# Kernel tuning notes

Hardware: AMD Instinct MI355X
Metric: run time of the kernel (lower is better)

Reference implementation:

```python
import jax, jax.numpy as jnp
import numpy as np

NEG_SLOPE = 0.2
N, IN_DIM, OUT_DIM, N_HEADS = 4096, 512, 512, 4
D_K = OUT_DIM // N_HEADS


def setup_inputs() -> dict:
    key = jax.random.key(0)
    k1, k2, k3, k4, k5 = jax.random.split(key, 5)
    H = jax.random.normal(k1, (N, IN_DIM), dtype=jnp.float32)
    A = jax.random.randint(k2, (N, N), 0, 2, dtype=jnp.int32)
    W = jax.random.normal(k3, (IN_DIM, OUT_DIM), dtype=jnp.float32) * (1.0 / np.sqrt(IN_DIM))
    a_l = jax.random.normal(k4, (N_HEADS, D_K), dtype=jnp.float32) * 0.1
    a_r = jax.random.normal(k5, (N_HEADS, D_K), dtype=jnp.float32) * 0.1
    return {"H": H, "A": A, "W": W, "a_l": a_l, "a_r": a_r}


def reference(H, A, W, a_l, a_r):
    n = H.shape[0]
    # mask = (A + I) > 0, shape (N, N); self-loops always allowed
    mask = (A + jnp.eye(n, dtype=A.dtype)) > 0
    # Wh: (N, heads, d_k)
    Wh = (H @ W).reshape(n, N_HEADS, D_K)
    sl = jnp.einsum('nhd,hd->nh', Wh, a_l)  # (N, heads)
    sr = jnp.einsum('nhd,hd->nh', Wh, a_r)  # (N, heads)
    # e[i, h, j] = leaky_relu(sl[i,h] + sr[j,h])
    e = jax.nn.leaky_relu(sl[:, :, None] + sr.T[None, :, :], negative_slope=NEG_SLOPE)
    e = jnp.where(mask[:, None, :], e, -jnp.inf)
    alpha = jnp.nan_to_num(jax.nn.softmax(e, axis=2), nan=0.0)  # dropout is identity at eval
    # out[i, h, :] = sum_j alpha[i,h,j] * Wh[j,h,:]
    out = jnp.einsum('nhm,mhd->nhd', alpha, Wh).reshape(n, OUT_DIM)
    return jax.nn.elu(out)
```

## Files before the change

kernel.cpp:

```cpp
#include <hip/hip_runtime.h>

typedef unsigned short ushort_t;
typedef __attribute__((ext_vector_type(8)))  short  short8;
typedef __attribute__((ext_vector_type(4)))  short  short4v;
typedef __attribute__((ext_vector_type(4)))  float  float4v;
typedef __attribute__((ext_vector_type(4)))  int    int4v;

#define N_NODES 4096
#define NHEADS  4
#define DK      128
#define ODIM    512
#define KDIM    512

__device__ __forceinline__ float bf2f(ushort_t u) {
    return __uint_as_float(((unsigned)u) << 16);
}
__device__ __forceinline__ ushort_t f2bf_rne(float f) {
    unsigned u = __float_as_uint(f);
    u += 0x7fffu + ((u >> 16) & 1u);
    return (ushort_t)(u >> 16);
}

__global__ __launch_bounds__(256) void pack_mask_k(const int* __restrict__ A,
                                                   unsigned long long* __restrict__ P,
                                                   const ushort_t* __restrict__ Hraw,
                                                   int* __restrict__ flag,
                                                   const void* __restrict__ W,
                                                   ushort_t* __restrict__ WT,
                                                   float* __restrict__ sl,
                                                   float* __restrict__ sr)
{
    __shared__ ushort_t lt[64][72];
    __shared__ int dcnt[4];
    const int tid = threadIdx.x;
    const int bx  = blockIdx.x;

    if (bx == 0 && tid < 64) {
        const int lane = tid;
        int cnt = 0;
        #pragma unroll
        for (int s = 0; s < 16; ++s) {
            ushort_t v = Hraw[(lane * 16 + s) * 2];
            int e = (v >> 7) & 0xFF;
            cnt += (((e >= 90) && (e <= 140)) || (v == 0)) ? 1 : 0;
        }
        #pragma unroll
        for (int off = 32; off; off >>= 1) cnt += __shfl_down(cnt, off);
        if (lane == 0) *flag = (cnt < 768) ? 1 : 0;
    }

    {
        const int lane  = tid & 63;
        const int flat4 = bx * 256 + tid;
        const int row   = flat4 >> 10;
        const int col0  = (flat4 << 2) & 4095;
        const int4v a   = ((const int4v*)A)[flat4];
        unsigned nib = 0;
        #pragma unroll
        for (int j = 0; j < 4; ++j)
            nib |= ((a[j] != 0) || (row == col0 + j)) ? (1u << j) : 0u;
        unsigned long long v = (unsigned long long)nib << ((lane & 15) * 4);
        v |= __shfl_xor(v, 1);
        v |= __shfl_xor(v, 2);
        v |= __shfl_xor(v, 4);
        v |= __shfl_xor(v, 8);
        if ((lane & 15) == 0) P[flat4 >> 4] = v;
    }

    if (bx >= 64 && bx < 96) {
        const int idx = (bx - 64) * 256 + tid;
        float4v z;
        #pragma unroll
        for (int e = 0; e < 4; ++e) z[e] = 0.f;
        if (idx < 4096) ((float4v*)sl)[idx] = z;
        else            ((float4v*)sr)[idx - 4096] = z;
    }

    if (bx < 64) {
        int cnt = 0;
        #pragma unroll
        for (int s = 0; s < 4; ++s) {
            ushort_t v = Hraw[(tid * 4 + s) * 2];
            int e = (v >> 7) & 0xFF;
            cnt += (((e >= 90) && (e <= 140)) || (v == 0)) ? 1 : 0;
        }
        #pragma unroll
        for (int off = 32; off; off >>= 1) cnt += __shfl_down(cnt, off);
        if ((tid & 63) == 0) dcnt[tid >> 6] = cnt;
        __syncthreads();
        const int f32 = (dcnt[0] + dcnt[1] + dcnt[2] + dcnt[3]) < 768;

        const int ti = bx >> 3, tj = bx & 7;
        const int r = tid >> 2, c2 = tid & 3;
        const size_t eo = (size_t)(ti * 64 + r) * KDIM + tj * 64 + c2 * 16;
        if (f32) {
            const float4v* src = (const float4v*)((const float*)W + eo);
            float4v f0 = src[0], f1 = src[1], f2 = src[2], f3 = src[3];
            #pragma unroll
            for (int e = 0; e < 4; ++e) {
                lt[r][c2 * 16 +  0 + e] = f2bf_rne(f0[e]);
                lt[r][c2 * 16 +  4 + e] = f2bf_rne(f1[e]);
                lt[r][c2 * 16 +  8 + e] = f2bf_rne(f2[e]);
                lt[r][c2 * 16 + 12 + e] = f2bf_rne(f3[e]);
            }
        } else {
            const short8* src = (const short8*)((const ushort_t*)W + eo);
            short8 v0 = src[0];
            short8 v1 = src[1];
            *(short8*)&lt[r][c2 * 16]     = v0;
            *(short8*)&lt[r][c2 * 16 + 8] = v1;
        }
        __syncthreads();
        #pragma unroll
        for (int itr = 0; itr < 2; ++itr) {
            int idx = itr * 256 + tid;
            int n = idx >> 3, c = idx & 7;
            short8 vv;
            #pragma unroll
            for (int e = 0; e < 8; ++e) vv[e] = (short)lt[c * 8 + e][n];
            *(short8*)(WT + (size_t)(tj * 64 + n) * KDIM + ti * 64 + c * 8) = vv;
        }
    }
}

__global__ __launch_bounds__(256) void gemm_wht_dual_k(const void* __restrict__ H,
                                                       const ushort_t* __restrict__ WT,
                                                       ushort_t* __restrict__ WhT,
                                                       const int* __restrict__ flag,
                                                       const void* __restrict__ al,
                                                       const void* __restrict__ ar,
                                                       float* __restrict__ sl,
                                                       float* __restrict__ sr)
{
    __shared__ ushort_t lt[64][72];
    const int f32 = *flag;
    const int tid  = threadIdx.x;
    const int lane = tid & 63;
    const int wid  = tid >> 6;
    const int quad = lane >> 4;
    const int l15  = lane & 15;
    const int bm = blockIdx.x & 63, bn = blockIdx.x >> 6;
    const int i0 = bm * 64, n0 = bn * 64;

    const size_t aoff = (size_t)(i0 + wid * 16 + l15) * KDIM + quad * 8;
    const short8* bp0 = (const short8*)(WT + (size_t)(n0 +  0 + l15) * KDIM) + quad;
    const short8* bp1 = (const short8*)(WT + (size_t)(n0 + 16 + l15) * KDIM) + quad;
    const short8* bp2 = (const short8*)(WT + (size_t)(n0 + 32 + l15) * KDIM) + quad;
    const short8* bp3 = (const short8*)(WT + (size_t)(n0 + 48 + l15) * KDIM) + quad;

    float4v acc0, acc1, acc2, acc3;
    #pragma unroll
    for (int e = 0; e < 4; ++e) { acc0[e] = 0.f; acc1[e] = 0.f; acc2[e] = 0.f; acc3[e] = 0.f; }

    #pragma unroll 4
    for (int k8 = 0; k8 < 64; k8 += 4) {
        short8 a;
        if (f32) {
            const float4v* fp = (const float4v*)((const float*)H + aoff + (size_t)k8 * 8);
            float4v x0 = fp[0], x1 = fp[1];
            #pragma unroll
            for (int e = 0; e < 4; ++e) {
                a[e]     = (short)f2bf_rne(x0[e]);
                a[4 + e] = (short)f2bf_rne(x1[e]);
            }
        } else {
            a = *(const short8*)((const ushort_t*)H + aoff + (size_t)k8 * 8);
        }
        acc0 = __builtin_amdgcn_mfma_f32_16x16x32_bf16(a, bp0[k8], acc0, 0, 0, 0);
        acc1 = __builtin_amdgcn_mfma_f32_16x16x32_bf16(a, bp1[k8], acc1, 0, 0, 0);
        acc2 = __builtin_amdgcn_mfma_f32_16x16x32_bf16(a, bp2[k8], acc2, 0, 0, 0);
        acc3 = __builtin_amdgcn_mfma_f32_16x16x32_bf16(a, bp3[k8], acc3, 0, 0, 0);
    }

    #pragma unroll
    for (int r = 0; r < 4; ++r) {
        int m = wid * 16 + quad * 4 + r;
        lt[ 0 + l15][m] = f2bf_rne(acc0[r]);
        lt[16 + l15][m] = f2bf_rne(acc1[r]);
        lt[32 + l15][m] = f2bf_rne(acc2[r]);
        lt[48 + l15][m] = f2bf_rne(acc3[r]);
    }
    __syncthreads();
    #pragma unroll
    for (int itr = 0; itr < 2; ++itr) {
        int idx = itr * 256 + tid;
        int n = idx >> 3, c = idx & 7;
        short8 v = *(const short8*)&lt[n][c * 8];
        *(short8*)(WhT + (size_t)(n0 + n) * N_NODES + i0 + c * 8) = v;
    }

    {
        const int h2 = n0 >> 7;
        const int d0 = n0 & 127;
        const int m  = tid >> 2;
        const int part = tid & 3;
        float psl = 0.f, psr = 0.f;
        #pragma unroll
        for (int k = 0; k < 16; ++k) {
            int n = part * 16 + k;
            float wv = bf2f(lt[n][m]);
            float av = f32 ? ((const float*)al)[h2 * DK + d0 + n]
                           : bf2f(((const ushort_t*)al)[h2 * DK + d0 + n]);
            float bv = f32 ? ((const float*)ar)[h2 * DK + d0 + n]
                           : bf2f(((const ushort_t*)ar)[h2 * DK + d0 + n]);
            psl += wv * av;
            psr += wv * bv;
        }
        psl += __shfl_down(psl, 2); psl += __shfl_down(psl, 1);
        psr += __shfl_down(psr, 2); psr += __shfl_down(psr, 1);
        if (part == 0) {
            atomicAdd(&sl[h2 * N_NODES + i0 + m], psl);
            atomicAdd(&sr[h2 * N_NODES + i0 + m], psr);
        }
    }
}

__global__ __launch_bounds__(256, 2) void attn_split_k(const ushort_t* __restrict__ WhT,
                                                       const unsigned* __restrict__ Apack,
                                                       const float* __restrict__ sl,
                                                       const float* __restrict__ sr,
                                                       float* __restrict__ Npart,
                                                       float* __restrict__ Dpart)
{
    __shared__ char smem[73728] __attribute__((aligned(16)));
    float*    srs  = (float*)smem;
    unsigned (*mbuf)[64] = (unsigned (*)[64])(smem + 8192);
    ushort_t* vbuf = (ushort_t*)(smem + 24576);

    const int tid  = threadIdx.x;
    const int lane = tid & 63;
    const int wq   = tid >> 6;
    const int quad = lane >> 4;
    const int l15  = lane & 15;
    const int bx   = blockIdx.x;
    const int half = bx & 1;
    const int h    = (bx >> 1) & 3;
    const int i0   = (bx >> 3) << 6;
    const int jbase = half << 11;

    const float C1 = 1.44269504f;

    for (int j = tid; j < 2048; j += 256) srs[j] = sr[h * N_NODES + jbase + j] * C1;
    for (int t = tid; t < 64 * 64; t += 256) {
        int r = t >> 6, c = t & 63;
        mbuf[r][c ^ r] = Apack[(size_t)(i0 + r) * 128 + (half << 6) + c];
    }
    const int myrow = wq * 16 + l15;
    const float slv = sl[h * N_NODES + i0 + myrow] * C1;
    __syncthreads();

    float4v acc[8];
    #pragma unroll
    for (int nt = 0; nt < 8; ++nt)
        #pragma unroll
        for (int e = 0; e < 4; ++e) acc[nt][e] = 0.f;
    float4v accden;
    #pragma unroll
    for (int e = 0; e < 4; ++e) accden[e] = 0.f;

    short8 ones;
    #pragma unroll
    for (int e = 0; e < 8; ++e) ones[e] = (short)0x3F80;

    const int dl  = lane >> 3;
    const int pch = (lane & 7) ^ (dl & 7);
    const ushort_t* g0 = WhT + (size_t)(h * DK + wq * 32 + dl) * N_NODES + jbase + pch * 8;

    #define DMA_WIN(BUF, IW)                                                         \
        {   ushort_t* lb_ = vbuf + (BUF) * 8192 + wq * 2048;                         \
            const ushort_t* gs_ = g0 + (IW) * 64;                                    \
            _Pragma("unroll")                                                        \
            for (int q_ = 0; q_ < 4; ++q_)                                           \
                __builtin_amdgcn_global_load_lds(                                    \
                    (const __attribute__((address_space(1))) void*)(gs_ + (size_t)q_ * 8 * N_NODES), \
                    (__attribute__((address_space(3))) void*)(lb_ + q_ * 512),       \
                    16, 0, 0);                                                       \
        }

    DMA_WIN(0, 0)
    DMA_WIN(1, 1)

    const int rs0 = (quad     ^ (l15 & 7)) * 8;
    const int rs1 = ((4 + quad) ^ (l15 & 7)) * 8;

    #pragma unroll 1
    for (int iw = 0; iw < 32; ++iw) {
        const int jl = iw * 64;

        const unsigned wa0 = mbuf[myrow][(iw * 2)     ^ myrow];
        const unsigned wa1 = mbuf[myrow][(iw * 2 + 1) ^ myrow];
        const float4v s0 = *(const float4v*)&srs[jl + quad * 8];
        const float4v s1 = *(const float4v*)&srs[jl + quad * 8 + 4];
        const float4v s2 = *(const float4v*)&srs[jl + 32 + quad * 8];
        const float4v s3 = *(const float4v*)&srs[jl + 32 + quad * 8 + 4];

        short8 pfA, pfB;
        #pragma unroll
        for (int jj = 0; jj < 8; ++jj) {
            const int bit = quad * 8 + jj;
            float srjA = (jj < 4) ? s0[jj] : s1[jj - 4];
            float xA = slv + srjA;
            float tA = fmaxf(xA, xA * 0.2f);
            tA = ((wa0 >> bit) & 1u) ? tA : -1e30f;
            pfA[jj] = (short)(ushort_t)(__float_as_uint(__builtin_amdgcn_exp2f(tA)) >> 16);
            float srjB = (jj < 4) ? s2[jj] : s3[jj - 4];
            float xB = slv + srjB;
            float tB = fmaxf(xB, xB * 0.2f);
            tB = ((wa1 >> bit) & 1u) ? tB : -1e30f;
            pfB[jj] = (short)(ushort_t)(__float_as_uint(__builtin_amdgcn_exp2f(tB)) >> 16);
        }

        if (iw == 31) { asm volatile("s_waitcnt vmcnt(0)" ::: "memory"); }
        else          { asm volatile("s_waitcnt vmcnt(4)" ::: "memory"); }
        asm volatile("s_barrier" ::: "memory");
        if (iw < 30) DMA_WIN((iw + 2) % 3, iw + 2)

        const ushort_t* vB = vbuf + (iw % 3) * 8192;
        #pragma unroll
        for (int nt = 0; nt < 8; ++nt) {
            const int d64 = (nt * 16 + l15) * 64;
            short8 b0 = *(const short8*)(vB + d64 + rs0);
            short8 b1 = *(const short8*)(vB + d64 + rs1);
            acc[nt] = __builtin_amdgcn_mfma_f32_16x16x32_bf16(pfA, b0, acc[nt], 0, 0, 0);
            acc[nt] = __builtin_amdgcn_mfma_f32_16x16x32_bf16(pfB, b1, acc[nt], 0, 0, 0);
        }
        accden = __builtin_amdgcn_mfma_f32_16x16x32_bf16(pfA, ones, accden, 0, 0, 0);
        accden = __builtin_amdgcn_mfma_f32_16x16x32_bf16(pfB, ones, accden, 0, 0, 0);
    }
    #undef DMA_WIN

    float* Np = Npart + (size_t)half * N_NODES * ODIM;
    #pragma unroll
    for (int nt = 0; nt < 8; ++nt)
        #pragma unroll
        for (int r = 0; r < 4; ++r) {
            const int rowi = wq * 16 + quad * 4 + r;
            Np[(size_t)(i0 + rowi) * ODIM + h * DK + nt * 16 + l15] = acc[nt][r];
        }
    if (l15 == 0) {
        #pragma unroll
        for (int r = 0; r < 4; ++r) {
            const int rowi = wq * 16 + quad * 4 + r;
            Dpart[(half * 4 + h) * N_NODES + i0 + rowi] = accden[r];
        }
    }
}

__global__ __launch_bounds__(256) void merge_k(const float* __restrict__ Npart,
                                               const float* __restrict__ Dpart,
                                               void* __restrict__ out,
                                               const int* __restrict__ flag)
{
    const int f32 = *flag;
    const size_t e4 = ((size_t)blockIdx.x * 256 + threadIdx.x) * 4;
    const int i = (int)(e4 >> 9);
    const int c = (int)(e4 & 511);
    const int h = c >> 7;
    const float4v n0 = *(const float4v*)(Npart + e4);
    const float4v n1 = *(const float4v*)(Npart + (size_t)N_NODES * ODIM + e4);
    const float den = Dpart[h * N_NODES + i] + Dpart[(4 + h) * N_NODES + i];
    const float rinv = 1.0f / fmaxf(den, 1e-37f);
    const float C1 = 1.44269504f;
    float o[4];
    #pragma unroll
    for (int k = 0; k < 4; ++k) {
        float v = (n0[k] + n1[k]) * rinv;
        float e = __builtin_amdgcn_exp2f(v * C1) - 1.0f;
        o[k] = (v > 0.f) ? v : e;
    }
    if (f32) {
        float4v ov;
        #pragma unroll
        for (int k = 0; k < 4; ++k) ov[k] = o[k];
        *(float4v*)((float*)out + e4) = ov;
    } else {
        short4v ov;
        #pragma unroll
        for (int k = 0; k < 4; ++k) ov[k] = (short)f2bf_rne(o[k]);
        *(short4v*)((ushort_t*)out + e4) = ov;
    }
}

__global__ __launch_bounds__(256, 2) void attn_single_k(const ushort_t* __restrict__ WhT,
                                                        const unsigned* __restrict__ Apack,
                                                        const float* __restrict__ sl,
                                                        const float* __restrict__ sr,
                                                        void* __restrict__ out,
                                                        const int* __restrict__ flag)
{
    __shared__ float    srs[N_NODES];
    __shared__ unsigned mbuf[32][128];
    __shared__ float    red[2][32][128];
    __shared__ float    lsum[4][32];

    const int f32  = *flag;
    const int tid  = threadIdx.x;
    const int lane = tid & 63;
    const int wq   = tid >> 6;
    const int quad = lane >> 4;
    const int l15  = lane & 15;
    const int h    = blockIdx.x & 3;
    const int i0   = (blockIdx.x >> 2) << 5;

    for (int j = tid; j < N_NODES; j += 256) srs[j] = sr[h * N_NODES + j];
    for (int t = tid; t < 32 * 128; t += 256) {
        int r = t >> 7, c = t & 127;
        mbuf[r][c] = Apack[(size_t)(i0 + r) * 128 + c];
    }
    const float slv0 = sl[h * N_NODES + i0 + l15];
    const float slv1 = sl[h * N_NODES + i0 + 16 + l15];
    __syncthreads();

    const float C1 = 1.44269504f;
    const float C2 = 0.2f * 1.44269504f;

    float4v acc[2][8];
    #pragma unroll
    for (int mg = 0; mg < 2; ++mg)
        #pragma unroll
        for (int nt = 0; nt < 8; ++nt)
            #pragma unroll
            for (int e = 0; e < 4; ++e) acc[mg][nt][e] = 0.f;
    float lacc0 = 0.f, lacc1 = 0.f;

    const ushort_t* vb = WhT + (size_t)(h * DK + l15) * N_NODES + wq * 1024 + quad * 8;

    #pragma unroll 1
    for (int it = 0; it < 16; ++it) {
        const int jl = it * 64;
        const int j0 = wq * 1024 + jl;
        const int mc = j0 >> 5;

        short8 bf[8][2];
        #pragma unroll
        for (int nt = 0; nt < 8; ++nt) {
            bf[nt][0] = *(const short8*)(vb + (size_t)nt * 16 * N_NODES + jl);
            bf[nt][1] = *(const short8*)(vb + (size_t)nt * 16 * N_NODES + jl + 32);
        }

        const unsigned wa0 = mbuf[l15][mc],      wa1 = mbuf[l15][mc + 1];
        const unsigned wb0 = mbuf[16 + l15][mc], wb1 = mbuf[16 + l15][mc + 1];

        short8 pf0[2], pf1[2];
        #pragma unroll
        for (int s = 0; s < 2; ++s) {
            const float* sp = &srs[j0 + s * 32 + quad * 8];
            const float4v s0 = *(const float4v*)sp;
            const float4v s1 = *(const float4v*)(sp + 4);
            const unsigned wa = s ? wa1 : wa0;
            const unsigned wb = s ? wb1 : wb0;
            #pragma unroll
            for (int jj = 0; jj < 8; ++jj) {
                float srj = (jj < 4) ? s0[jj] : s1[jj - 4];
                int bit = quad * 8 + jj;
                float x0 = slv0 + srj;
                float t0 = fmaxf(x0 * C1, x0 * C2);
                t0 = ((wa >> bit) & 1u) ? t0 : -1e30f;
                float p0 = __builtin_amdgcn_exp2f(t0);
                ushort_t h0 = (ushort_t)(__float_as_uint(p0) >> 16);
                lacc0 += bf2f(h0);
                pf0[s][jj] = (short)h0;
                float x1 = slv1 + srj;
                float t1 = fmaxf(x1 * C1, x1 * C2);
                t1 = ((wb >> bit) & 1u) ? t1 : -1e30f;
                float p1 = __builtin_amdgcn_exp2f(t1);
                ushort_t h1 = (ushort_t)(__float_as_uint(p1) >> 16);
                lacc1 += bf2f(h1);
                pf1[s][jj] = (short)h1;
            }
        }

        #pragma unroll
        for (int nt = 0; nt < 8; ++nt) {
            acc[0][nt] = __builtin_amdgcn_mfma_f32_16x16x32_bf16(pf0[0], bf[nt][0], acc[0][nt], 0, 0, 0);
            acc[0][nt] = __builtin_amdgcn_mfma_f32_16x16x32_bf16(pf0[1], bf[nt][1], acc[0][nt], 0, 0, 0);
            acc[1][nt] = __builtin_amdgcn_mfma_f32_16x16x32_bf16(pf1[0], bf[nt][0], acc[1][nt], 0, 0, 0);
            acc[1][nt] = __builtin_amdgcn_mfma_f32_16x16x32_bf16(pf1[1], bf[nt][1], acc[1][nt], 0, 0, 0);
        }
    }

    lacc0 += __shfl_xor(lacc0, 16);
    lacc0 += __shfl_xor(lacc0, 32);
    lacc1 += __shfl_xor(lacc1, 16);
    lacc1 += __shfl_xor(lacc1, 32);
    if (lane < 16) {
        lsum[wq][l15]      = lacc0;
        lsum[wq][16 + l15] = lacc1;
    }
    if (wq >= 2) {
        #pragma unroll
        for (int mg = 0; mg < 2; ++mg)
            #pragma unroll
            for (int nt = 0; nt < 8; ++nt)
                #pragma unroll
                for (int r = 0; r < 4; ++r)
                    red[wq - 2][mg * 16 + quad * 4 + r][nt * 16 + l15] = acc[mg][nt][r];
    }
    __syncthreads();
    if (wq < 2) {
        #pragma unroll
        for (int mg = 0; mg < 2; ++mg)
            #pragma unroll
            for (int nt = 0; nt < 8; ++nt)
                #pragma unroll
                for (int r = 0; r < 4; ++r)
                    acc[mg][nt][r] += red[wq][mg * 16 + quad * 4 + r][nt * 16 + l15];
    }
    __syncthreads();
    if (wq == 1) {
        #pragma unroll
        for (int mg = 0; mg < 2; ++mg)
            #pragma unroll
            for (int nt = 0; nt < 8; ++nt)
                #pragma unroll
                for (int r = 0; r < 4; ++r)
                    red[0][mg * 16 + quad * 4 + r][nt * 16 + l15] = acc[mg][nt][r];
    }
    __syncthreads();
    if (wq == 0) {
        #pragma unroll
        for (int mg = 0; mg < 2; ++mg) {
            float linv[4];
            #pragma unroll
            for (int r = 0; r < 4; ++r) {
                int rowi = mg * 16 + quad * 4 + r;
                float den = lsum[0][rowi] + lsum[1][rowi] + lsum[2][rowi] + lsum[3][rowi];
                linv[r] = 1.0f / fmaxf(den, 1e-37f);
            }
            #pragma unroll
            for (int nt = 0; nt < 8; ++nt)
                #pragma unroll
                for (int r = 0; r < 4; ++r) {
                    int rowi = mg * 16 + quad * 4 + r;
                    float v = (acc[mg][nt][r] + red[0][rowi][nt * 16 + l15]) * linv[r];
                    float e = __builtin_amdgcn_exp2f(v * C1) - 1.0f;
                    float o = (v > 0.f) ? v : e;
                    size_t oidx = (size_t)(i0 + rowi) * ODIM + h * DK + nt * 16 + l15;
                    if (f32) ((float*)out)[oidx] = o;
                    else     ((ushort_t*)out)[oidx] = f2bf_rne(o);
                }
        }
    }
}

extern "C" void kernel_launch(void* const* d_in, const int* in_sizes, int n_in,
                              void* d_out, int out_size, void* d_ws, size_t ws_size,
                              hipStream_t stream)
{
    const void* H  = d_in[0];
    const int*  A  = (const int*)d_in[1];
    const void* W  = d_in[2];
    const void* al = d_in[3];
    const void* ar = d_in[4];

    if (ws_size < (7u << 20)) return;

    char* ws = (char*)d_ws;
    ushort_t* WhT   = (ushort_t*)ws;
    unsigned long long* Apack = (unsigned long long*)(ws + (4u << 20));
    ushort_t* WT    = (ushort_t*)(ws + (6u << 20));
    float*    sl    = (float*)(ws + (6u << 20) + (512u << 10));
    float*    sr    = (float*)(ws + (6u << 20) + (576u << 10));
    int*      flag  = (int*)(ws + (6u << 20) + (640u << 10));
    float*    Npart = (float*)(ws + (12u << 20));
    float*    Dpart = (float*)(ws + (28u << 20));
    const bool have_split = ws_size >= (29u << 20);

    pack_mask_k    <<<16384, 256, 0, stream>>>(A, Apack, (const ushort_t*)H, flag,
                                               W, WT, sl, sr);
    gemm_wht_dual_k<<<512,   256, 0, stream>>>(H, WT, WhT, flag, al, ar, sl, sr);
    if (have_split) {
        attn_split_k<<<512, 256, 0, stream>>>(WhT, (const unsigned*)Apack, sl, sr, Npart, Dpart);
        merge_k     <<<2048, 256, 0, stream>>>(Npart, Dpart, (void*)d_out, flag);
    } else {
        attn_single_k<<<512, 256, 0, stream>>>(WhT, (const unsigned*)Apack, sl, sr, (void*)d_out, flag);
    }
}
```

Baseline: 174.0 us.

## Split attention j-range across two wave groups per block with LDS reduction

Doubles the attention block to 512 threads. Two groups of four waves each handle half of the block's 2048-column j range, using 32-column windows with a new swizzle and a triple-buffered DMA per group. At the end the two groups' partial numerators and denominators are summed through LDS. This aims to raise the number of waves in flight to hide latency, at the cost of a final reduction, an extra barrier, and register pressure under the (512,4) launch bounds.

```diff
diff --git a/kernel.cpp b/kernel.cpp
--- a/kernel.cpp
+++ b/kernel.cpp
@@ -215,7 +215,7 @@
     }
 }
 
-__global__ __launch_bounds__(256, 2) void attn_split_k(const ushort_t* __restrict__ WhT,
+__global__ __launch_bounds__(512, 4) void attn_split_k(const ushort_t* __restrict__ WhT,
                                                        const unsigned* __restrict__ Apack,
                                                        const float* __restrict__ sl,
                                                        const float* __restrict__ sr,
@@ -229,7 +229,9 @@
 
     const int tid  = threadIdx.x;
     const int lane = tid & 63;
-    const int wq   = tid >> 6;
+    const int wid  = tid >> 6;
+    const int wq   = wid & 3;
+    const int js   = wid >> 2;
     const int quad = lane >> 4;
     const int l15  = lane & 15;
     const int bx   = blockIdx.x;
@@ -240,8 +242,8 @@
 
     const float C1 = 1.44269504f;
 
-    for (int j = tid; j < 2048; j += 256) srs[j] = sr[h * N_NODES + jbase + j] * C1;
-    for (int t = tid; t < 64 * 64; t += 256) {
+    for (int j = tid; j < 2048; j += 512) srs[j] = sr[h * N_NODES + jbase + j] * C1;
+    for (int t = tid; t < 64 * 64; t += 512) {
         int r = t >> 6, c = t & 63;
         mbuf[r][c ^ r] = Apack[(size_t)(i0 + r) * 128 + (half << 6) + c];
     }
@@ -262,17 +264,18 @@
     #pragma unroll
     for (int e = 0; e < 8; ++e) ones[e] = (short)0x3F80;
 
-    const int dl  = lane >> 3;
-    const int pch = (lane & 7) ^ (dl & 7);
-    const ushort_t* g0 = WhT + (size_t)(h * DK + wq * 32 + dl) * N_NODES + jbase + pch * 8;
+    const int dl  = lane >> 2;
+    const int gch = (lane & 3) ^ (dl & 3) ^ ((dl >> 2) & 1);
+    const ushort_t* g0 = WhT + (size_t)(h * DK + wq * 32 + dl) * N_NODES
+                             + jbase + js * 1024 + gch * 8;
 
     #define DMA_WIN(BUF, IW)                                                         \
-        {   ushort_t* lb_ = vbuf + (BUF) * 8192 + wq * 2048;                         \
-            const ushort_t* gs_ = g0 + (IW) * 64;                                    \
+        {   ushort_t* lb_ = vbuf + js * 12288 + (BUF) * 4096 + wq * 1024;            \
+            const ushort_t* gs_ = g0 + (IW) * 32;                                    \
             _Pragma("unroll")                                                        \
-            for (int q_ = 0; q_ < 4; ++q_)                                           \
+            for (int q_ = 0; q_ < 2; ++q_)                                           \
                 __builtin_amdgcn_global_load_lds(                                    \
-                    (const __attribute__((address_space(1))) void*)(gs_ + (size_t)q_ * 8 * N_NODES), \
+                    (const __attribute__((address_space(1))) void*)(gs_ + (size_t)q_ * 16 * N_NODES), \
                     (__attribute__((address_space(3))) void*)(lb_ + q_ * 512),       \
                     16, 0, 0);                                                       \
         }
@@ -280,68 +283,74 @@
     DMA_WIN(0, 0)
     DMA_WIN(1, 1)
 
-    const int rs0 = (quad     ^ (l15 & 7)) * 8;
-    const int rs1 = ((4 + quad) ^ (l15 & 7)) * 8;
+    const int rs = (quad ^ (l15 & 3) ^ ((l15 >> 2) & 1)) * 8;
 
     #pragma unroll 1
     for (int iw = 0; iw < 32; ++iw) {
-        const int jl = iw * 64;
-
-        const unsigned wa0 = mbuf[myrow][(iw * 2)     ^ myrow];
-        const unsigned wa1 = mbuf[myrow][(iw * 2 + 1) ^ myrow];
-        const float4v s0 = *(const float4v*)&srs[jl + quad * 8];
-        const float4v s1 = *(const float4v*)&srs[jl + quad * 8 + 4];
-        const float4v s2 = *(const float4v*)&srs[jl + 32 + quad * 8];
-        const float4v s3 = *(const float4v*)&srs[jl + 32 + quad * 8 + 4];
-
-        short8 pfA, pfB;
+        const unsigned wa = mbuf[myrow][(js * 32 + iw) ^ myrow];
+        const float4v s0 = *(const float4v*)&srs[js * 1024 + iw * 32 + quad * 8];
+        const float4v s1 = *(const float4v*)&srs[js * 1024 + iw * 32 + quad * 8 + 4];
+
+        short8 pf;
         #pragma unroll
         for (int jj = 0; jj < 8; ++jj) {
             const int bit = quad * 8 + jj;
-            float srjA = (jj < 4) ? s0[jj] : s1[jj - 4];
-            float xA = slv + srjA;
-            float tA = fmaxf(xA, xA * 0.2f);
-            tA = ((wa0 >> bit) & 1u) ? tA : -1e30f;
-            pfA[jj] = (short)(ushort_t)(__float_as_uint(__builtin_amdgcn_exp2f(tA)) >> 16);
-            float srjB = (jj < 4) ? s2[jj] : s3[jj - 4];
-            float xB = slv + srjB;
-            float tB = fmaxf(xB, xB * 0.2f);
-            tB = ((wa1 >> bit) & 1u) ? tB : -1e30f;
-            pfB[jj] = (short)(ushort_t)(__float_as_uint(__builtin_amdgcn_exp2f(tB)) >> 16);
+            float srj = (jj < 4) ? s0[jj] : s1[jj - 4];
+            float x = slv + srj;
+            float t = fmaxf(x, x * 0.2f);
+            t = ((wa >> bit) & 1u) ? t : -1e30f;
+            pf[jj] = (short)(ushort_t)(__float_as_uint(__builtin_amdgcn_exp2f(t)) >> 16);
         }
 
         if (iw == 31) { asm volatile("s_waitcnt vmcnt(0)" ::: "memory"); }
-        else          { asm volatile("s_waitcnt vmcnt(4)" ::: "memory"); }
+        else          { asm volatile("s_waitcnt vmcnt(2)" ::: "memory"); }
         asm volatile("s_barrier" ::: "memory");
         if (iw < 30) DMA_WIN((iw + 2) % 3, iw + 2)
 
-        const ushort_t* vB = vbuf + (iw % 3) * 8192;
+        const ushort_t* vB = vbuf + js * 12288 + (iw % 3) * 4096;
         #pragma unroll
         for (int nt = 0; nt < 8; ++nt) {
-            const int d64 = (nt * 16 + l15) * 64;
-            short8 b0 = *(const short8*)(vB + d64 + rs0);
-            short8 b1 = *(const short8*)(vB + d64 + rs1);
-            acc[nt] = __builtin_amdgcn_mfma_f32_16x16x32_bf16(pfA, b0, acc[nt], 0, 0, 0);
-            acc[nt] = __builtin_amdgcn_mfma_f32_16x16x32_bf16(pfB, b1, acc[nt], 0, 0, 0);
-        }
-        accden = __builtin_amdgcn_mfma_f32_16x16x32_bf16(pfA, ones, accden, 0, 0, 0);
-        accden = __builtin_amdgcn_mfma_f32_16x16x32_bf16(pfB, ones, accden, 0, 0, 0);
+            short8 b = *(const short8*)(vB + (nt * 16 + l15) * 32 + rs);
+            acc[nt] = __builtin_amdgcn_mfma_f32_16x16x32_bf16(pf, b, acc[nt], 0, 0, 0);
+        }
+        accden = __builtin_amdgcn_mfma_f32_16x16x32_bf16(pf, ones, accden, 0, 0, 0);
     }
     #undef DMA_WIN
 
-    float* Np = Npart + (size_t)half * N_NODES * ODIM;
-    #pragma unroll
-    for (int nt = 0; nt < 8; ++nt)
-        #pragma unroll
-        for (int r = 0; r < 4; ++r) {
-            const int rowi = wq * 16 + quad * 4 + r;
-            Np[(size_t)(i0 + rowi) * ODIM + h * DK + nt * 16 + l15] = acc[nt][r];
-        }
-    if (l15 == 0) {
-        #pragma unroll
-        for (int r = 0; r < 4; ++r) {
-            const int rowi = wq * 16 + quad * 4 + r;
-            Dpart[(half * 4 + h) * N_NODES + i0 + rowi] = accden[r];
+    float* red  = (float*)(smem + 24576);
+    float* lsum = (float*)(smem + 24576 + 32768);
+    __syncthreads();
+
+    if (js == 1) {
+        #pragma unroll
+        for (int nt = 0; nt < 8; ++nt)
+            #pragma unroll
+            for (int r = 0; r < 4; ++r)
+                red[wq * 2048 + (quad * 4 + r) * 128 + nt * 16 + l15] = acc[nt][r];
+        if (l15 == 0) {
+            #pragma unroll
+            for (int r = 0; r < 4; ++r)
+                lsum[wq * 16 + quad * 4 + r] = accden[r];
+        }
+    }
+    __syncthreads();
+    if (js == 0) {
+        float* Np = Npart + (size_t)half * N_NODES * ODIM;
+        #pragma unroll
+        for (int nt = 0; nt < 8; ++nt)
+            #pragma unroll
+            for (int r = 0; r < 4; ++r) {
+                const int rowi = wq * 16 + quad * 4 + r;
+                float v = acc[nt][r] + red[wq * 2048 + (quad * 4 + r) * 128 + nt * 16 + l15];
+                Np[(size_t)(i0 + rowi) * ODIM + h * DK + nt * 16 + l15] = v;
+            }
+        if (l15 == 0) {
+            #pragma unroll
+            for (int r = 0; r < 4; ++r) {
+                const int rowi = wq * 16 + quad * 4 + r;
+                Dpart[(half * 4 + h) * N_NODES + i0 + rowi] =
+                    accden[r] + lsum[wq * 16 + quad * 4 + r];
+            }
         }
     }
 }
@@ -570,7 +579,7 @@
                                                W, WT, sl, sr);
     gemm_wht_dual_k<<<512,   256, 0, stream>>>(H, WT, WhT, flag, al, ar, sl, sr);
     if (have_split) {
-        attn_split_k<<<512, 256, 0, stream>>>(WhT, (const unsigned*)Apack, sl, sr, Npart, Dpart);
+        attn_split_k<<<512, 512, 0, stream>>>(WhT, (const unsigned*)Apack, sl, sr, Npart, Dpart);
         merge_k     <<<2048, 256, 0, stream>>>(Npart, Dpart, (void*)d_out, flag);
     } else {
         attn_single_k<<<512, 256, 0, stream>>>(WhT, (const unsigned*)Apack, sl, sr, (void*)d_out, flag);
```

Result: faster. 169.7 us (-2.5%).
